# Kernel optimization log

Measured on AMD Instinct MI355X. Metric: run time of the kernel, lower is better.

## Reference

```python
import jax, jax.numpy as jnp
from jax import lax
import numpy as np

VOCAB, TAGS, EMB, HID = 50000, 45, 256, 512
B, S = 32, 256


def setup_inputs() -> dict:
    key = jax.random.key(0)
    ks = jax.random.split(key, 12)
    sc = 0.05
    return {
        "x": jax.random.randint(ks[0], (B, S), 0, VOCAB),
        "tags": jax.random.randint(ks[1], (B, S), 0, TAGS),
        "emb": jax.random.normal(ks[2], (VOCAB, EMB), jnp.float32) * sc,
        "w_ih_f": jax.random.normal(ks[3], (4 * HID, EMB), jnp.float32) * sc,
        "w_hh_f": jax.random.normal(ks[4], (4 * HID, HID), jnp.float32) * sc,
        "b_f": jnp.zeros((4 * HID,), jnp.float32),
        "w_ih_b": jax.random.normal(ks[5], (4 * HID, EMB), jnp.float32) * sc,
        "w_hh_b": jax.random.normal(ks[6], (4 * HID, HID), jnp.float32) * sc,
        "b_b": jnp.zeros((4 * HID,), jnp.float32),
        "lin_w": jax.random.normal(ks[7], (TAGS, 2 * HID), jnp.float32) * sc,
        "lin_b": jnp.zeros((TAGS,), jnp.float32),
        "start_t": jax.random.normal(ks[8], (TAGS,), jnp.float32) * 0.1,
        "end_t": jax.random.normal(ks[9], (TAGS,), jnp.float32) * 0.1,
        "trans": jax.random.normal(ks[10], (TAGS,), jnp.float32)[:, None] * 0.0 + jax.random.normal(ks[11], (TAGS, TAGS), jnp.float32) * 0.1,
    }


def _lstm_dir(xs, w_ih, w_hh, b, reverse):
    # xs: [B,S,E]. PyTorch gate order: i, f, g, o.
    Bsz = xs.shape[0]
    H = w_hh.shape[1]
    def step(carry, x_t):
        h, c = carry
        g = x_t @ w_ih.T + h @ w_hh.T + b
        i, f, gg, o = jnp.split(g, 4, axis=-1)
        c = jax.nn.sigmoid(f) * c + jax.nn.sigmoid(i) * jnp.tanh(gg)
        h = jax.nn.sigmoid(o) * jnp.tanh(c)
        return (h, c), h
    init = (jnp.zeros((Bsz, H), xs.dtype), jnp.zeros((Bsz, H), xs.dtype))
    _, hs = lax.scan(step, init, jnp.swapaxes(xs, 0, 1), reverse=reverse)
    return jnp.swapaxes(hs, 0, 1)  # [B,S,H]


def _crf_nll(em, tags, start_t, end_t, trans):
    # em: [B,S,T]; numerator: score of gold path
    em_sc = jnp.take_along_axis(em, tags[..., None], axis=2)[..., 0].sum(axis=1)
    tr_sc = trans[tags[:, :-1], tags[:, 1:]].sum(axis=1)
    score = start_t[tags[:, 0]] + em_sc + tr_sc + end_t[tags[:, -1]]
    # partition function via forward algorithm (logsumexp recurrence)
    alpha0 = start_t + em[:, 0]  # [B,T]
    def step(alpha, e_t):
        alpha = jax.nn.logsumexp(alpha[:, :, None] + trans[None], axis=1) + e_t
        return alpha, None
    alpha, _ = lax.scan(step, alpha0, jnp.swapaxes(em[:, 1:], 0, 1))
    logZ = jax.nn.logsumexp(alpha + end_t, axis=1)
    return -(score - logZ).mean()  # reduction='mean', loss = -llh


def reference(x, tags, emb, w_ih_f, w_hh_f, b_f, w_ih_b, w_hh_b, b_b,
              lin_w, lin_b, start_t, end_t, trans):
    embeds = emb[x]                               # [B,S,E]
    h_f = _lstm_dir(embeds, w_ih_f, w_hh_f, b_f, False)
    h_b = _lstm_dir(embeds, w_ih_b, w_hh_b, b_b, True)
    lstm_out = jnp.concatenate([h_f, h_b], axis=-1)  # [B,S,2H]
    emissions = lstm_out @ lin_w.T + lin_b           # [B,S,T]
    return _crf_nll(emissions, tags, start_t, end_t, trans)
```

## Files before the change

kernel.cpp:

```cpp
#include <hip/hip_runtime.h>

#define BB 32
#define SS 256
#define EMBD 256
#define HIDD 512
#define NTAG 45
#define TPAD 48
#define NBLK 16
#define APAD 520
#define GRID_REC 32
#define GSTR 130
#define SENT 0x01010101u

typedef __bf16 bf16x8 __attribute__((ext_vector_type(8)));
typedef float  f32x4  __attribute__((ext_vector_type(4)));
typedef short  s16x8  __attribute__((ext_vector_type(8)));
typedef unsigned u32x4 __attribute__((ext_vector_type(4)));

__device__ __forceinline__ unsigned short f2bf(float x) {
  unsigned u = __builtin_bit_cast(unsigned, x);
  u = (u + 0x7fffu + ((u >> 16) & 1u)) >> 16;
  return (unsigned short)u;
}
__device__ __forceinline__ float bf2f(unsigned short u) {
  unsigned v = ((unsigned)u) << 16; return __builtin_bit_cast(float, v);
}
__device__ __forceinline__ float fsig(float x) {
  float e = __builtin_amdgcn_exp2f(-1.44269504f * x);
  return __builtin_amdgcn_rcpf(1.f + e);
}
__device__ __forceinline__ float ftanh(float x) {
  float e = __builtin_amdgcn_exp2f(-2.88539008f * x);
  return 2.f * __builtin_amdgcn_rcpf(1.f + e) - 1.f;
}

__device__ __forceinline__ void st64_sys(unsigned* p, unsigned a, unsigned b) {
  unsigned long long v = ((unsigned long long)b << 32) | (unsigned long long)a;
  asm volatile("global_store_dwordx2 %0, %1, off sc0 sc1" :: "v"(p), "v"(v) : "memory");
}

#define LD8(CPOL)                                                           \
  asm volatile("global_load_dwordx4 %0, %[q0], off " CPOL "\n\t"            \
               "global_load_dwordx4 %1, %[q1], off " CPOL "\n\t"            \
               "global_load_dwordx4 %2, %[q2], off " CPOL "\n\t"            \
               "global_load_dwordx4 %3, %[q3], off " CPOL "\n\t"            \
               "global_load_dwordx4 %4, %[q4], off " CPOL "\n\t"            \
               "global_load_dwordx4 %5, %[q5], off " CPOL "\n\t"            \
               "global_load_dwordx4 %6, %[q6], off " CPOL "\n\t"            \
               "global_load_dwordx4 %7, %[q7], off " CPOL "\n\t"            \
               "s_waitcnt vmcnt(0)"                                         \
               : "=&v"(v0), "=&v"(v1), "=&v"(v2), "=&v"(v3),                \
                 "=&v"(v4), "=&v"(v5), "=&v"(v6), "=&v"(v7)                 \
               : [q0] "v"(p), [q1] "v"(p + 2048), [q2] "v"(p + 4096),       \
                 [q3] "v"(p + 6144), [q4] "v"(p + 8192), [q5] "v"(p + 10240),\
                 [q6] "v"(p + 12288), [q7] "v"(p + 14336)                   \
               : "memory")

__global__ void k_pack_e(const int* __restrict__ x, const float* __restrict__ emb,
                         unsigned short* __restrict__ E) {
  int idx = blockIdx.x * 256 + threadIdx.x;
  int e = idx & 255; int bt = idx >> 8; int b = bt & 31; int t = bt >> 5;
  int tok = x[b * SS + t];
  E[idx] = f2bf(emb[(long)tok * EMBD + e]);
}

__global__ void k_pack_w(const float* __restrict__ wih_f, const float* __restrict__ whh_f,
                         const float* __restrict__ bf_,  const float* __restrict__ wih_b,
                         const float* __restrict__ whh_b, const float* __restrict__ bb_,
                         unsigned short* __restrict__ Wh, unsigned short* __restrict__ Wie,
                         float* __restrict__ Bh) {
  long idx = (long)blockIdx.x * 256 + threadIdx.x;
  int k = (int)(idx % 768); long rest = idx / 768;
  int r2 = (int)(rest & 2047); int dir = (int)(rest >> 11);
  int blk = r2 >> 6, rl = r2 & 63, gate = rl >> 4, hl = rl & 15;
  int orig = gate * HIDD + blk * 16 + hl;
  const float* wih = dir ? wih_b : wih_f;
  const float* whh = dir ? whh_b : whh_f;
  if (k < HIDD) Wh[((long)(dir * 2048 + r2)) * 512 + k] = f2bf(whh[(long)orig * HIDD + k]);
  else          Wie[((long)(dir * 2048 + r2)) * 256 + (k - 512)] = f2bf(wih[(long)orig * EMBD + (k - 512)]);
  if (k == 0) {
    const float* bias = dir ? bb_ : bf_;
    Bh[dir * 2048 + r2] = bias[orig];
  }
}

__global__ void k_pack_l(const float* __restrict__ lin_w, const float* __restrict__ lin_b,
                         unsigned short* __restrict__ LW, float* __restrict__ LB) {
  int idx = blockIdx.x * 256 + threadIdx.x;
  if (idx < TPAD * 1024) {
    int tag = idx >> 10; int c = idx & 1023;
    LW[idx] = (tag < NTAG) ? f2bf(lin_w[tag * 1024 + c]) : (unsigned short)0;
  } else if (idx < TPAD * 1024 + TPAD) {
    int tag = idx - TPAD * 1024;
    LB[tag] = (tag < NTAG) ? lin_b[tag] : 0.f;
  }
}

__launch_bounds__(256)
__global__ void k_eproj(const unsigned short* __restrict__ E,
                        const unsigned short* __restrict__ Wie,
                        const float* __restrict__ Bh,
                        unsigned short* __restrict__ Ep) {
  __shared__ unsigned short W2[64 * 264];
  const int bx = blockIdx.x;
  const int tg = bx & 63, blk = (bx >> 6) & 31, dir = bx >> 11;
  const int tid = threadIdx.x;
  const int w = tid >> 6, lane = tid & 63;
  const int lm = lane & 15, quad = lane >> 4;

  {
    const unsigned short* src = Wie + ((long)(dir * 2048 + blk * 64)) * 256;
    for (int i = 0; i < 8; ++i) {
      int c = i * 256 + tid;
      int row = c >> 5, off = c & 31;
      *(s16x8*)&W2[row * 264 + off * 8] = *(const s16x8*)&src[row * 256 + off * 8];
    }
  }
  __syncthreads();

  f32x4 acc[2][4] = {};
#pragma unroll
  for (int kk = 0; kk < 8; ++kk) {
    s16x8 av[2];
#pragma unroll
    for (int sub = 0; sub < 2; ++sub)
      av[sub] = *(const s16x8*)&E[((long)(tg * 128 + w * 32 + sub * 16 + lm)) * 256 + kk * 32 + quad * 8];
#pragma unroll
    for (int sub = 0; sub < 2; ++sub)
#pragma unroll
      for (int n = 0; n < 4; ++n) {
        s16x8 bs = *(const s16x8*)&W2[(n * 16 + lm) * 264 + kk * 32 + quad * 8];
        acc[sub][n] = __builtin_amdgcn_mfma_f32_16x16x32_bf16(
            __builtin_bit_cast(bf16x8, av[sub]), __builtin_bit_cast(bf16x8, bs), acc[sub][n], 0, 0, 0);
      }
  }
  float bh[4];
#pragma unroll
  for (int n = 0; n < 4; ++n) bh[n] = Bh[dir * 2048 + blk * 64 + n * 16 + lm];
#pragma unroll
  for (int sub = 0; sub < 2; ++sub)
#pragma unroll
    for (int n = 0; n < 4; ++n)
#pragma unroll
      for (int r = 0; r < 4; ++r) {
        int m = w * 32 + sub * 16 + quad * 4 + r;
        int t = tg * 4 + (m >> 5), b = m & 31;
        int row_l = n * 16 + lm;
        Ep[((((long)(dir * 32 + blk) * 256 + t) * 32 + b) * 64) + row_l] =
            f2bf(acc[sub][n][r] + bh[n]);
      }
}

__launch_bounds__(256, 1)
__global__ void k_rec(const unsigned short* __restrict__ Wh,
                      const unsigned short* __restrict__ Ep,
                      unsigned short* __restrict__ H) {
  __shared__ unsigned short A_ls[32 * APAD];
  __shared__ float G_ls[32 * GSTR];

  const int bx = blockIdx.x;
  const int dir = bx & 1;
  const int blk = bx >> 1;
  const int tid = threadIdx.x;
  const int w = tid >> 6, lane = tid & 63;
  const int lm = lane & 15, quad = lane >> 4;

  s16x8 wb[2][16];
  {
    const unsigned short* wsrc =
        Wh + ((long)(dir * 2048 + blk * 128 + w * 32 + lm)) * 512 + quad * 8;
#pragma unroll
    for (int ns = 0; ns < 2; ++ns)
#pragma unroll
      for (int kk = 0; kk < 16; ++kk)
        wb[ns][kk] = *(const s16x8*)&wsrc[ns * 16 * 512 + kk * 32];
  }

  const int m_act = tid >> 3, cg = tid & 7;
  float cst[4] = {0.f, 0.f, 0.f, 0.f};

  unsigned short* Hd = H + (long)dir * SS * BB * HIDD;
  const unsigned short* Epw =
      Ep + ((long)(dir * 32 + 2 * blk + (w >> 1)) * 256) * 32 * 64;
  const int ep_col = (w & 1) * 32 + lm;

  for (int t = 0; t < SS; ++t) {
    const int tE = (dir == 0) ? t : (SS - 1 - t);

    unsigned short epv[16];
    {
      const unsigned short* eb = Epw + ((long)tE * 32 + quad * 4) * 64 + ep_col;
#pragma unroll
      for (int mt = 0; mt < 2; ++mt)
#pragma unroll
        for (int ns = 0; ns < 2; ++ns)
#pragma unroll
          for (int r = 0; r < 4; ++r)
            epv[mt * 8 + ns * 4 + r] = eb[(mt * 16 + r) * 64 + ns * 16];
    }

    f32x4 acc[2][2] = {};
    if (t > 0) {
      {
        const int hslot = (dir == 0) ? (t - 1) : (SS - t);
        const unsigned short* p = Hd + (long)hslot * BB * HIDD + w * 512 + lane * 8;
        s16x8 v0, v1, v2, v3, v4, v5, v6, v7;
        unsigned bad;
        do {
          LD8("sc0 sc1");
          u32x4 u0 = __builtin_bit_cast(u32x4, v0), u1 = __builtin_bit_cast(u32x4, v1);
          u32x4 u2 = __builtin_bit_cast(u32x4, v2), u3 = __builtin_bit_cast(u32x4, v3);
          u32x4 u4 = __builtin_bit_cast(u32x4, v4), u5 = __builtin_bit_cast(u32x4, v5);
          u32x4 u6 = __builtin_bit_cast(u32x4, v6), u7 = __builtin_bit_cast(u32x4, v7);
          unsigned b0 = (u0.x == SENT) | (u0.y == SENT) | (u0.z == SENT) | (u0.w == SENT);
          unsigned b1 = (u1.x == SENT) | (u1.y == SENT) | (u1.z == SENT) | (u1.w == SENT);
          unsigned b2 = (u2.x == SENT) | (u2.y == SENT) | (u2.z == SENT) | (u2.w == SENT);
          unsigned b3 = (u3.x == SENT) | (u3.y == SENT) | (u3.z == SENT) | (u3.w == SENT);
          unsigned b4 = (u4.x == SENT) | (u4.y == SENT) | (u4.z == SENT) | (u4.w == SENT);
          unsigned b5 = (u5.x == SENT) | (u5.y == SENT) | (u5.z == SENT) | (u5.w == SENT);
          unsigned b6 = (u6.x == SENT) | (u6.y == SENT) | (u6.z == SENT) | (u6.w == SENT);
          unsigned b7 = (u7.x == SENT) | (u7.y == SENT) | (u7.z == SENT) | (u7.w == SENT);
          bad = (b0 | b1) | (b2 | b3) | ((b4 | b5) | (b6 | b7));
        } while (__builtin_expect(bad != 0u, 0));
        unsigned short* d = &A_ls[w * APAD + lane * 8];
        *(s16x8*)(d + 0 * 2080) = v0; *(s16x8*)(d + 1 * 2080) = v1;
        *(s16x8*)(d + 2 * 2080) = v2; *(s16x8*)(d + 3 * 2080) = v3;
        *(s16x8*)(d + 4 * 2080) = v4; *(s16x8*)(d + 5 * 2080) = v5;
        *(s16x8*)(d + 6 * 2080) = v6; *(s16x8*)(d + 7 * 2080) = v7;
      }
      __syncthreads();
#pragma unroll
      for (int kk = 0; kk < 16; ++kk) {
        s16x8 av0 = *(const s16x8*)&A_ls[(lm)      * APAD + kk * 32 + quad * 8];
        s16x8 av1 = *(const s16x8*)&A_ls[(16 + lm) * APAD + kk * 32 + quad * 8];
        acc[0][0] = __builtin_amdgcn_mfma_f32_16x16x32_bf16(
            __builtin_bit_cast(bf16x8, av0), __builtin_bit_cast(bf16x8, wb[0][kk]), acc[0][0], 0, 0, 0);
        acc[0][1] = __builtin_amdgcn_mfma_f32_16x16x32_bf16(
            __builtin_bit_cast(bf16x8, av0), __builtin_bit_cast(bf16x8, wb[1][kk]), acc[0][1], 0, 0, 0);
        acc[1][0] = __builtin_amdgcn_mfma_f32_16x16x32_bf16(
            __builtin_bit_cast(bf16x8, av1), __builtin_bit_cast(bf16x8, wb[0][kk]), acc[1][0], 0, 0, 0);
        acc[1][1] = __builtin_amdgcn_mfma_f32_16x16x32_bf16(
            __builtin_bit_cast(bf16x8, av1), __builtin_bit_cast(bf16x8, wb[1][kk]), acc[1][1], 0, 0, 0);
      }
    }
#pragma unroll
    for (int mt = 0; mt < 2; ++mt)
#pragma unroll
      for (int ns = 0; ns < 2; ++ns)
#pragma unroll
        for (int r = 0; r < 4; ++r) {
          int mm = mt * 16 + quad * 4 + r;
          G_ls[mm * GSTR + w * 32 + ns * 16 + lm] =
              acc[mt][ns][r] + bf2f(epv[mt * 8 + ns * 4 + r]);
        }
    __syncthreads();
    {
      float hv[4];
#pragma unroll
      for (int j = 0; j < 4; ++j) {
        int c = cg * 4 + j, sub = c >> 4, hl = c & 15;
        const float* gp = &G_ls[m_act * GSTR + sub * 64 + hl];
        float si = fsig(gp[0]);
        float sf = fsig(gp[16]);
        float tg = ftanh(gp[32]);
        float so = fsig(gp[48]);
        cst[j] = sf * cst[j] + si * tg;
        hv[j] = so * ftanh(cst[j]);
      }
      int tslot = (dir == 0) ? t : (SS - 1 - t);
      unsigned d0 = (unsigned)f2bf(hv[0]) | ((unsigned)f2bf(hv[1]) << 16);
      unsigned d1 = (unsigned)f2bf(hv[2]) | ((unsigned)f2bf(hv[3]) << 16);
      st64_sys((unsigned*)&Hd[(long)tslot * BB * HIDD + (long)m_act * HIDD + blk * 32 + cg * 4],
               d0, d1);
    }
  }
}

__launch_bounds__(256)
__global__ void k_emis(const unsigned short* __restrict__ H,
                       const unsigned short* __restrict__ LW,
                       const float* __restrict__ LB,
                       float* __restrict__ EM) {
  const int row0 = blockIdx.x * 32;
  const int tid = threadIdx.x;
  const int w = tid >> 6, lane = tid & 63;
  const int lm = lane & 15, quad = lane >> 4;
  const unsigned short* Hf = H;
  const unsigned short* Hb = H + (long)SS * BB * HIDD;

  for (int tile = w; tile < 6; tile += 4) {
    int mt = tile / 3, nt = tile % 3;
    int arow = row0 + mt * 16 + lm;
    int nrow = nt * 16 + lm;
    f32x4 acc = {0.f, 0.f, 0.f, 0.f};
#pragma unroll 4
    for (int kk = 0; kk < 32; ++kk) {
      int k0 = kk * 32 + quad * 8;
      s16x8 asv = (k0 < HIDD) ? *(const s16x8*)&Hf[(long)arow * HIDD + k0]
                              : *(const s16x8*)&Hb[(long)arow * HIDD + (k0 - HIDD)];
      s16x8 bsv = *(const s16x8*)&LW[nrow * 1024 + k0];
      acc = __builtin_amdgcn_mfma_f32_16x16x32_bf16(
          __builtin_bit_cast(bf16x8, asv), __builtin_bit_cast(bf16x8, bsv), acc, 0, 0, 0);
    }
    float bias = LB[nrow];
#pragma unroll
    for (int r = 0; r < 4; ++r) {
      int mm = row0 + mt * 16 + quad * 4 + r;
      EM[(long)mm * TPAD + nrow] = acc[r] + bias;
    }
  }
}

__global__ void k_crf(const int* __restrict__ tags, const float* __restrict__ start_t,
                      const float* __restrict__ end_t, const float* __restrict__ trans,
                      const float* __restrict__ EM, float* __restrict__ chain) {
  __shared__ float T_ls[NTAG * TPAD];
  __shared__ float ET[48 * 48 + 16];
  __shared__ float P_ls[64];
  const int b = blockIdx.x;
  const int lane = threadIdx.x;
  const int j = lane;

  for (int i = lane; i < NTAG * NTAG; i += 64)
    T_ls[(i / NTAG) * TPAD + (i % NTAG)] = trans[i];
  for (int i = lane; i < 48 * 48 + 16; i += 64) ET[i] = 0.f;
  __syncthreads();

  float Mj = -1e30f;
  if (j < NTAG) {
    for (int i = 0; i < NTAG; ++i) Mj = fmaxf(Mj, T_ls[i * TPAD + j]);
    for (int i = 0; i < NTAG; ++i) ET[i * 48 + j] = __expf(T_ls[i * TPAD + j] - Mj);
  }
  __syncthreads();

  float et[48];
#pragma unroll
  for (int i = 0; i < 48; ++i) et[i] = ET[i * 48 + j];

  float part = 0.f;
  for (int t = lane; t < SS; t += 64) {
    int tg = tags[b * SS + t];
    part += EM[((long)t * BB + b) * TPAD + tg];
    if (t + 1 < SS) part += T_ls[tg * TPAD + tags[b * SS + t + 1]];
    if (t == 0)      part += start_t[tg];
    if (t == SS - 1) part += end_t[tg];
  }
  for (int off = 32; off; off >>= 1) part += __shfl_down(part, off);
  float score = __shfl(part, 0);

  float alpha = (j < NTAG) ? (start_t[j] + EM[(long)b * TPAD + j]) : -1e30f;
  float e_next = (j < NTAG) ? EM[((long)BB + b) * TPAD + j] : 0.f;
  for (int t = 1; t < SS; ++t) {
    float e_cur = e_next;
    if (t < SS - 1) e_next = (j < NTAG) ? EM[((long)(t + 1) * BB + b) * TPAD + j] : 0.f;
    float am = alpha;
#pragma unroll
    for (int off = 32; off; off >>= 1) am = fmaxf(am, __shfl_xor(am, off));
    float p = __expf(alpha - am);
    P_ls[lane] = p;
    __builtin_amdgcn_wave_barrier();
    float s0 = 0.f, s1 = 0.f, s2 = 0.f, s3 = 0.f;
#pragma unroll
    for (int i0 = 0; i0 < 48; i0 += 4) {
      f32x4 pv = *(const f32x4*)&P_ls[i0];
      s0 += pv.x * et[i0];
      s1 += pv.y * et[i0 + 1];
      s2 += pv.z * et[i0 + 2];
      s3 += pv.w * et[i0 + 3];
    }
    __builtin_amdgcn_wave_barrier();
    float s = (s0 + s1) + (s2 + s3);
    float na = am + Mj + __logf(s) + e_cur;
    alpha = (j < NTAG) ? na : -1e30f;
  }
  float v = (j < NTAG) ? (alpha + end_t[j]) : -1e30f;
  float mx = v;
  for (int off = 32; off; off >>= 1) mx = fmaxf(mx, __shfl_xor(mx, off));
  float s = __expf(v - mx);
  for (int off = 32; off; off >>= 1) s += __shfl_xor(s, off);
  if (lane == 0) chain[b] = score - (mx + __logf(s));
}

__global__ void k_fin(const float* __restrict__ chain, float* __restrict__ out) {
  int lane = threadIdx.x;
  float v = (lane < BB) ? chain[lane] : 0.f;
  for (int off = 32; off; off >>= 1) v += __shfl_xor(v, off);
  if (lane == 0) out[0] = -v / (float)BB;
}

extern "C" void kernel_launch(void* const* d_in, const int* in_sizes, int n_in,
                              void* d_out, int out_size, void* d_ws, size_t ws_size,
                              hipStream_t stream) {
  const int*   x      = (const int*)d_in[0];
  const int*   tags   = (const int*)d_in[1];
  const float* emb    = (const float*)d_in[2];
  const float* wih_f  = (const float*)d_in[3];
  const float* whh_f  = (const float*)d_in[4];
  const float* b_f    = (const float*)d_in[5];
  const float* wih_b  = (const float*)d_in[6];
  const float* whh_b  = (const float*)d_in[7];
  const float* b_b    = (const float*)d_in[8];
  const float* lin_w  = (const float*)d_in[9];
  const float* lin_b  = (const float*)d_in[10];
  const float* start_t= (const float*)d_in[11];
  const float* end_t  = (const float*)d_in[12];
  const float* trans  = (const float*)d_in[13];

  char* ws = (char*)d_ws;
  size_t off = 0;
  auto alloc = [&](size_t bytes) {
    void* p = ws + off; off = (off + bytes + 255) & ~(size_t)255; return p;
  };
  unsigned short* E   = (unsigned short*)alloc((size_t)SS * BB * EMBD * 2);
  unsigned short* Wh  = (unsigned short*)alloc((size_t)2 * 2048 * 512 * 2);
  unsigned short* Wie = (unsigned short*)alloc((size_t)2 * 2048 * 256 * 2);
  float*          Bh  = (float*)         alloc((size_t)2 * 2048 * 4);
  unsigned short* Ep  = (unsigned short*)alloc((size_t)2 * 32 * 256 * 32 * 64 * 2);
  unsigned short* H   = (unsigned short*)alloc((size_t)2 * SS * BB * HIDD * 2);
  unsigned short* LW  = (unsigned short*)alloc((size_t)TPAD * 1024 * 2);
  float*          LB  = (float*)         alloc((size_t)TPAD * 4);
  float*          EM  = (float*)         alloc((size_t)SS * BB * TPAD * 4);
  float*          chain = (float*)       alloc((size_t)BB * 4);

  hipMemsetAsync(H, 0x01, (size_t)2 * SS * BB * HIDD * 2, stream);
  k_pack_e<<<dim3((SS * BB * EMBD) / 256), dim3(256), 0, stream>>>(x, emb, E);
  k_pack_w<<<dim3((2 * 2048 * 768) / 256), dim3(256), 0, stream>>>(
      wih_f, whh_f, b_f, wih_b, whh_b, b_b, Wh, Wie, Bh);
  k_pack_l<<<dim3((TPAD * 1024 + TPAD + 255) / 256), dim3(256), 0, stream>>>(
      lin_w, lin_b, LW, LB);
  k_eproj<<<dim3(4096), dim3(256), 0, stream>>>(E, Wie, Bh, Ep);

  void* kargs[] = {&Wh, &Ep, &H};
  hipLaunchCooperativeKernel((const void*)k_rec, dim3(GRID_REC), dim3(256), kargs, 0, stream);

  k_emis<<<dim3((SS * BB) / 32), dim3(256), 0, stream>>>(H, LW, LB, EM);
  k_crf<<<dim3(BB), dim3(64), 0, stream>>>(tags, start_t, end_t, trans, EM, chain);
  k_fin<<<dim3(1), dim3(64), 0, stream>>>(chain, (float*)d_out);
}
```

Baseline: 1.083 ms.

## Fuse input projection into recurrent kernel and merge packing kernels

Removes the separate input-projection kernel and its Ep buffer, and instead computes the x·W_ih product inside each recurrent step from register-resident W_ih slices and the packed embeddings. The hidden-state load is restructured so each wave polls its own A-operand fragments directly from global memory and feeds them into MFMA, which drops the LDS staging and one barrier per step. The gate buffer is double-buffered, and the three pack kernels are merged into one launch. This trades the global Ep round-trip and extra launches for more MFMA work and register pressure on the serial critical path, plus finer-grained sentinel polling.

```diff
diff --git a/kernel.cpp b/kernel.cpp
--- a/kernel.cpp
+++ b/kernel.cpp
@@ -7,7 +7,6 @@
 #define NTAG 45
 #define TPAD 48
 #define NBLK 16
-#define APAD 520
 #define GRID_REC 32
 #define GSTR 130
 #define SENT 0x01010101u
@@ -22,9 +21,6 @@
   u = (u + 0x7fffu + ((u >> 16) & 1u)) >> 16;
   return (unsigned short)u;
 }
-__device__ __forceinline__ float bf2f(unsigned short u) {
-  unsigned v = ((unsigned)u) << 16; return __builtin_bit_cast(float, v);
-}
 __device__ __forceinline__ float fsig(float x) {
   float e = __builtin_amdgcn_exp2f(-1.44269504f * x);
   return __builtin_amdgcn_rcpf(1.f + e);
@@ -33,130 +29,76 @@
   float e = __builtin_amdgcn_exp2f(-2.88539008f * x);
   return 2.f * __builtin_amdgcn_rcpf(1.f + e) - 1.f;
 }
+__device__ __forceinline__ f32x4 MF(s16x8 a, s16x8 b, f32x4 c) {
+  return __builtin_amdgcn_mfma_f32_16x16x32_bf16(
+      __builtin_bit_cast(bf16x8, a), __builtin_bit_cast(bf16x8, b), c, 0, 0, 0);
+}
+__device__ __forceinline__ unsigned has_sent(s16x8 v) {
+  u32x4 u = __builtin_bit_cast(u32x4, v);
+  return (unsigned)((u.x == SENT) | (u.y == SENT) | (u.z == SENT) | (u.w == SENT));
+}
 
 __device__ __forceinline__ void st64_sys(unsigned* p, unsigned a, unsigned b) {
   unsigned long long v = ((unsigned long long)b << 32) | (unsigned long long)a;
   asm volatile("global_store_dwordx2 %0, %1, off sc0 sc1" :: "v"(p), "v"(v) : "memory");
 }
-
-#define LD8(CPOL)                                                           \
-  asm volatile("global_load_dwordx4 %0, %[q0], off " CPOL "\n\t"            \
-               "global_load_dwordx4 %1, %[q1], off " CPOL "\n\t"            \
-               "global_load_dwordx4 %2, %[q2], off " CPOL "\n\t"            \
-               "global_load_dwordx4 %3, %[q3], off " CPOL "\n\t"            \
-               "global_load_dwordx4 %4, %[q4], off " CPOL "\n\t"            \
-               "global_load_dwordx4 %5, %[q5], off " CPOL "\n\t"            \
-               "global_load_dwordx4 %6, %[q6], off " CPOL "\n\t"            \
-               "global_load_dwordx4 %7, %[q7], off " CPOL "\n\t"            \
-               "s_waitcnt vmcnt(0)"                                         \
-               : "=&v"(v0), "=&v"(v1), "=&v"(v2), "=&v"(v3),                \
-                 "=&v"(v4), "=&v"(v5), "=&v"(v6), "=&v"(v7)                 \
-               : [q0] "v"(p), [q1] "v"(p + 2048), [q2] "v"(p + 4096),       \
-                 [q3] "v"(p + 6144), [q4] "v"(p + 8192), [q5] "v"(p + 10240),\
-                 [q6] "v"(p + 12288), [q7] "v"(p + 14336)                   \
-               : "memory")
-
-__global__ void k_pack_e(const int* __restrict__ x, const float* __restrict__ emb,
-                         unsigned short* __restrict__ E) {
-  int idx = blockIdx.x * 256 + threadIdx.x;
-  int e = idx & 255; int bt = idx >> 8; int b = bt & 31; int t = bt >> 5;
-  int tok = x[b * SS + t];
-  E[idx] = f2bf(emb[(long)tok * EMBD + e]);
-}
-
-__global__ void k_pack_w(const float* __restrict__ wih_f, const float* __restrict__ whh_f,
-                         const float* __restrict__ bf_,  const float* __restrict__ wih_b,
-                         const float* __restrict__ whh_b, const float* __restrict__ bb_,
-                         unsigned short* __restrict__ Wh, unsigned short* __restrict__ Wie,
-                         float* __restrict__ Bh) {
-  long idx = (long)blockIdx.x * 256 + threadIdx.x;
-  int k = (int)(idx % 768); long rest = idx / 768;
-  int r2 = (int)(rest & 2047); int dir = (int)(rest >> 11);
-  int blk = r2 >> 6, rl = r2 & 63, gate = rl >> 4, hl = rl & 15;
-  int orig = gate * HIDD + blk * 16 + hl;
-  const float* wih = dir ? wih_b : wih_f;
-  const float* whh = dir ? whh_b : whh_f;
-  if (k < HIDD) Wh[((long)(dir * 2048 + r2)) * 512 + k] = f2bf(whh[(long)orig * HIDD + k]);
-  else          Wie[((long)(dir * 2048 + r2)) * 256 + (k - 512)] = f2bf(wih[(long)orig * EMBD + (k - 512)]);
-  if (k == 0) {
-    const float* bias = dir ? bb_ : bf_;
-    Bh[dir * 2048 + r2] = bias[orig];
-  }
-}
-
-__global__ void k_pack_l(const float* __restrict__ lin_w, const float* __restrict__ lin_b,
-                         unsigned short* __restrict__ LW, float* __restrict__ LB) {
-  int idx = blockIdx.x * 256 + threadIdx.x;
-  if (idx < TPAD * 1024) {
-    int tag = idx >> 10; int c = idx & 1023;
-    LW[idx] = (tag < NTAG) ? f2bf(lin_w[tag * 1024 + c]) : (unsigned short)0;
-  } else if (idx < TPAD * 1024 + TPAD) {
-    int tag = idx - TPAD * 1024;
-    LB[tag] = (tag < NTAG) ? lin_b[tag] : 0.f;
-  }
-}
-
-__launch_bounds__(256)
-__global__ void k_eproj(const unsigned short* __restrict__ E,
-                        const unsigned short* __restrict__ Wie,
-                        const float* __restrict__ Bh,
-                        unsigned short* __restrict__ Ep) {
-  __shared__ unsigned short W2[64 * 264];
-  const int bx = blockIdx.x;
-  const int tg = bx & 63, blk = (bx >> 6) & 31, dir = bx >> 11;
+#define LDH2()                                                          \
+  asm volatile("global_load_dwordx4 %0, %2, off sc0 sc1\n\t"            \
+               "global_load_dwordx4 %1, %3, off sc0 sc1\n\t"            \
+               "s_waitcnt vmcnt(0)"                                     \
+               : "=&v"(a0), "=&v"(a1) : "v"(p0), "v"(p1) : "memory")
+
+#define NB_W 12288
+#define NB_E 8192
+#define NB_L 193
+__global__ void k_pack(const int* __restrict__ x, const float* __restrict__ emb,
+                       const float* __restrict__ wih_f, const float* __restrict__ whh_f,
+                       const float* __restrict__ bf_,  const float* __restrict__ wih_b,
+                       const float* __restrict__ whh_b, const float* __restrict__ bb_,
+                       const float* __restrict__ lin_w, const float* __restrict__ lin_b,
+                       unsigned short* __restrict__ E,  unsigned short* __restrict__ Wh,
+                       unsigned short* __restrict__ Wie, float* __restrict__ Bh,
+                       unsigned short* __restrict__ LW, float* __restrict__ LB) {
+  const int bxg = blockIdx.x;
   const int tid = threadIdx.x;
-  const int w = tid >> 6, lane = tid & 63;
-  const int lm = lane & 15, quad = lane >> 4;
-
-  {
-    const unsigned short* src = Wie + ((long)(dir * 2048 + blk * 64)) * 256;
-    for (int i = 0; i < 8; ++i) {
-      int c = i * 256 + tid;
-      int row = c >> 5, off = c & 31;
-      *(s16x8*)&W2[row * 264 + off * 8] = *(const s16x8*)&src[row * 256 + off * 8];
-    }
-  }
-  __syncthreads();
-
-  f32x4 acc[2][4] = {};
-#pragma unroll
-  for (int kk = 0; kk < 8; ++kk) {
-    s16x8 av[2];
-#pragma unroll
-    for (int sub = 0; sub < 2; ++sub)
-      av[sub] = *(const s16x8*)&E[((long)(tg * 128 + w * 32 + sub * 16 + lm)) * 256 + kk * 32 + quad * 8];
-#pragma unroll
-    for (int sub = 0; sub < 2; ++sub)
-#pragma unroll
-      for (int n = 0; n < 4; ++n) {
-        s16x8 bs = *(const s16x8*)&W2[(n * 16 + lm) * 264 + kk * 32 + quad * 8];
-        acc[sub][n] = __builtin_amdgcn_mfma_f32_16x16x32_bf16(
-            __builtin_bit_cast(bf16x8, av[sub]), __builtin_bit_cast(bf16x8, bs), acc[sub][n], 0, 0, 0);
-      }
-  }
-  float bh[4];
-#pragma unroll
-  for (int n = 0; n < 4; ++n) bh[n] = Bh[dir * 2048 + blk * 64 + n * 16 + lm];
-#pragma unroll
-  for (int sub = 0; sub < 2; ++sub)
-#pragma unroll
-    for (int n = 0; n < 4; ++n)
-#pragma unroll
-      for (int r = 0; r < 4; ++r) {
-        int m = w * 32 + sub * 16 + quad * 4 + r;
-        int t = tg * 4 + (m >> 5), b = m & 31;
-        int row_l = n * 16 + lm;
-        Ep[((((long)(dir * 32 + blk) * 256 + t) * 32 + b) * 64) + row_l] =
-            f2bf(acc[sub][n][r] + bh[n]);
-      }
+  if (bxg < NB_W) {
+    long idx = (long)bxg * 256 + tid;
+    int k = (int)(idx % 768); long rest = idx / 768;
+    int r2 = (int)(rest & 2047); int dir = (int)(rest >> 11);
+    int blk = r2 >> 6, rl = r2 & 63, gate = rl >> 4, hl = rl & 15;
+    int orig = gate * HIDD + blk * 16 + hl;
+    const float* wih = dir ? wih_b : wih_f;
+    const float* whh = dir ? whh_b : whh_f;
+    if (k < HIDD) Wh[((long)(dir * 2048 + r2)) * 512 + k] = f2bf(whh[(long)orig * HIDD + k]);
+    else          Wie[((long)(dir * 2048 + r2)) * 256 + (k - 512)] = f2bf(wih[(long)orig * EMBD + (k - 512)]);
+    if (k == 0) {
+      const float* bias = dir ? bb_ : bf_;
+      Bh[dir * 2048 + r2] = bias[orig];
+    }
+  } else if (bxg < NB_W + NB_E) {
+    int idx = (bxg - NB_W) * 256 + tid;
+    int e = idx & 255; int bt = idx >> 8; int b = bt & 31; int t = bt >> 5;
+    int tok = x[b * SS + t];
+    E[idx] = f2bf(emb[(long)tok * EMBD + e]);
+  } else {
+    int idx = (bxg - NB_W - NB_E) * 256 + tid;
+    if (idx < TPAD * 1024) {
+      int tag = idx >> 10; int c = idx & 1023;
+      LW[idx] = (tag < NTAG) ? f2bf(lin_w[tag * 1024 + c]) : (unsigned short)0;
+    } else if (idx < TPAD * 1024 + TPAD) {
+      int tag = idx - TPAD * 1024;
+      LB[tag] = (tag < NTAG) ? lin_b[tag] : 0.f;
+    }
+  }
 }
 
 __launch_bounds__(256, 1)
 __global__ void k_rec(const unsigned short* __restrict__ Wh,
-                      const unsigned short* __restrict__ Ep,
+                      const unsigned short* __restrict__ Wie,
+                      const float* __restrict__ Bh,
+                      const unsigned short* __restrict__ E,
                       unsigned short* __restrict__ H) {
-  __shared__ unsigned short A_ls[32 * APAD];
-  __shared__ float G_ls[32 * GSTR];
+  __shared__ float G_ls[2][32 * GSTR];
 
   const int bx = blockIdx.x;
   const int dir = bx & 1;
@@ -165,84 +107,64 @@
   const int w = tid >> 6, lane = tid & 63;
   const int lm = lane & 15, quad = lane >> 4;
 
-  s16x8 wb[2][16];
+  s16x8 wb[2][16], wie[2][8];
+  float bh[2];
   {
-    const unsigned short* wsrc =
-        Wh + ((long)(dir * 2048 + blk * 128 + w * 32 + lm)) * 512 + quad * 8;
-#pragma unroll
-    for (int ns = 0; ns < 2; ++ns)
-#pragma unroll
-      for (int kk = 0; kk < 16; ++kk)
-        wb[ns][kk] = *(const s16x8*)&wsrc[ns * 16 * 512 + kk * 32];
+    const long rbase = (long)(dir * 2048 + blk * 128 + w * 32 + lm);
+#pragma unroll
+    for (int ns = 0; ns < 2; ++ns) {
+      const unsigned short* wsrc = Wh + (rbase + ns * 16) * 512 + quad * 8;
+#pragma unroll
+      for (int kk = 0; kk < 16; ++kk) wb[ns][kk] = *(const s16x8*)&wsrc[kk * 32];
+      const unsigned short* wesrc = Wie + (rbase + ns * 16) * 256 + quad * 8;
+#pragma unroll
+      for (int kk = 0; kk < 8; ++kk) wie[ns][kk] = *(const s16x8*)&wesrc[kk * 32];
+      bh[ns] = Bh[rbase + ns * 16];
+    }
   }
 
   const int m_act = tid >> 3, cg = tid & 7;
   float cst[4] = {0.f, 0.f, 0.f, 0.f};
 
   unsigned short* Hd = H + (long)dir * SS * BB * HIDD;
-  const unsigned short* Epw =
-      Ep + ((long)(dir * 32 + 2 * blk + (w >> 1)) * 256) * 32 * 64;
-  const int ep_col = (w & 1) * 32 + lm;
 
   for (int t = 0; t < SS; ++t) {
     const int tE = (dir == 0) ? t : (SS - 1 - t);
-
-    unsigned short epv[16];
+    f32x4 acc[2][2] = {};
+
     {
-      const unsigned short* eb = Epw + ((long)tE * 32 + quad * 4) * 64 + ep_col;
-#pragma unroll
-      for (int mt = 0; mt < 2; ++mt)
-#pragma unroll
-        for (int ns = 0; ns < 2; ++ns)
-#pragma unroll
-          for (int r = 0; r < 4; ++r)
-            epv[mt * 8 + ns * 4 + r] = eb[(mt * 16 + r) * 64 + ns * 16];
-    }
-
-    f32x4 acc[2][2] = {};
+      const unsigned short* eb = E + ((long)tE * BB) * EMBD + quad * 8;
+#pragma unroll
+      for (int kk = 0; kk < 8; ++kk) {
+        s16x8 e0 = *(const s16x8*)&eb[(long)lm * EMBD + kk * 32];
+        s16x8 e1 = *(const s16x8*)&eb[(long)(16 + lm) * EMBD + kk * 32];
+        acc[0][0] = MF(e0, wie[0][kk], acc[0][0]);
+        acc[0][1] = MF(e0, wie[1][kk], acc[0][1]);
+        acc[1][0] = MF(e1, wie[0][kk], acc[1][0]);
+        acc[1][1] = MF(e1, wie[1][kk], acc[1][1]);
+      }
+    }
+
     if (t > 0) {
-      {
-        const int hslot = (dir == 0) ? (t - 1) : (SS - t);
-        const unsigned short* p = Hd + (long)hslot * BB * HIDD + w * 512 + lane * 8;
-        s16x8 v0, v1, v2, v3, v4, v5, v6, v7;
-        unsigned bad;
-        do {
-          LD8("sc0 sc1");
-          u32x4 u0 = __builtin_bit_cast(u32x4, v0), u1 = __builtin_bit_cast(u32x4, v1);
-          u32x4 u2 = __builtin_bit_cast(u32x4, v2), u3 = __builtin_bit_cast(u32x4, v3);
-          u32x4 u4 = __builtin_bit_cast(u32x4, v4), u5 = __builtin_bit_cast(u32x4, v5);
-          u32x4 u6 = __builtin_bit_cast(u32x4, v6), u7 = __builtin_bit_cast(u32x4, v7);
-          unsigned b0 = (u0.x == SENT) | (u0.y == SENT) | (u0.z == SENT) | (u0.w == SENT);
-          unsigned b1 = (u1.x == SENT) | (u1.y == SENT) | (u1.z == SENT) | (u1.w == SENT);
-          unsigned b2 = (u2.x == SENT) | (u2.y == SENT) | (u2.z == SENT) | (u2.w == SENT);
-          unsigned b3 = (u3.x == SENT) | (u3.y == SENT) | (u3.z == SENT) | (u3.w == SENT);
-          unsigned b4 = (u4.x == SENT) | (u4.y == SENT) | (u4.z == SENT) | (u4.w == SENT);
-          unsigned b5 = (u5.x == SENT) | (u5.y == SENT) | (u5.z == SENT) | (u5.w == SENT);
-          unsigned b6 = (u6.x == SENT) | (u6.y == SENT) | (u6.z == SENT) | (u6.w == SENT);
-          unsigned b7 = (u7.x == SENT) | (u7.y == SENT) | (u7.z == SENT) | (u7.w == SENT);
-          bad = (b0 | b1) | (b2 | b3) | ((b4 | b5) | (b6 | b7));
-        } while (__builtin_expect(bad != 0u, 0));
-        unsigned short* d = &A_ls[w * APAD + lane * 8];
-        *(s16x8*)(d + 0 * 2080) = v0; *(s16x8*)(d + 1 * 2080) = v1;
-        *(s16x8*)(d + 2 * 2080) = v2; *(s16x8*)(d + 3 * 2080) = v3;
-        *(s16x8*)(d + 4 * 2080) = v4; *(s16x8*)(d + 5 * 2080) = v5;
-        *(s16x8*)(d + 6 * 2080) = v6; *(s16x8*)(d + 7 * 2080) = v7;
+      const int hslot = (dir == 0) ? (t - 1) : (SS - t);
+      const unsigned short* hb = Hd + (long)hslot * BB * HIDD + quad * 8;
+#pragma unroll 4
+      for (int kk = 0; kk < 16; ++kk) {
+        const unsigned short* p0 = hb + (long)lm * HIDD + kk * 32;
+        const unsigned short* p1 = hb + (long)(16 + lm) * HIDD + kk * 32;
+        s16x8 a0, a1;
+        for (;;) {
+          LDH2();
+          if (!(has_sent(a0) | has_sent(a1))) break;
+        }
+        acc[0][0] = MF(a0, wb[0][kk], acc[0][0]);
+        acc[0][1] = MF(a0, wb[1][kk], acc[0][1]);
+        acc[1][0] = MF(a1, wb[0][kk], acc[1][0]);
+        acc[1][1] = MF(a1, wb[1][kk], acc[1][1]);
       }
-      __syncthreads();
-#pragma unroll
-      for (int kk = 0; kk < 16; ++kk) {
-        s16x8 av0 = *(const s16x8*)&A_ls[(lm)      * APAD + kk * 32 + quad * 8];
-        s16x8 av1 = *(const s16x8*)&A_ls[(16 + lm) * APAD + kk * 32 + quad * 8];
-        acc[0][0] = __builtin_amdgcn_mfma_f32_16x16x32_bf16(
-            __builtin_bit_cast(bf16x8, av0), __builtin_bit_cast(bf16x8, wb[0][kk]), acc[0][0], 0, 0, 0);
-        acc[0][1] = __builtin_amdgcn_mfma_f32_16x16x32_bf16(
-            __builtin_bit_cast(bf16x8, av0), __builtin_bit_cast(bf16x8, wb[1][kk]), acc[0][1], 0, 0, 0);
-        acc[1][0] = __builtin_amdgcn_mfma_f32_16x16x32_bf16(
-            __builtin_bit_cast(bf16x8, av1), __builtin_bit_cast(bf16x8, wb[0][kk]), acc[1][0], 0, 0, 0);
-        acc[1][1] = __builtin_amdgcn_mfma_f32_16x16x32_bf16(
-            __builtin_bit_cast(bf16x8, av1), __builtin_bit_cast(bf16x8, wb[1][kk]), acc[1][1], 0, 0, 0);
-      }
-    }
+    }
+
+    float* G = G_ls[t & 1];
 #pragma unroll
     for (int mt = 0; mt < 2; ++mt)
 #pragma unroll
@@ -250,8 +172,7 @@
 #pragma unroll
         for (int r = 0; r < 4; ++r) {
           int mm = mt * 16 + quad * 4 + r;
-          G_ls[mm * GSTR + w * 32 + ns * 16 + lm] =
-              acc[mt][ns][r] + bf2f(epv[mt * 8 + ns * 4 + r]);
+          G[mm * GSTR + w * 32 + ns * 16 + lm] = acc[mt][ns][r] + bh[ns];
         }
     __syncthreads();
     {
@@ -259,7 +180,7 @@
 #pragma unroll
       for (int j = 0; j < 4; ++j) {
         int c = cg * 4 + j, sub = c >> 4, hl = c & 15;
-        const float* gp = &G_ls[m_act * GSTR + sub * 64 + hl];
+        const float* gp = &G[m_act * GSTR + sub * 64 + hl];
         float si = fsig(gp[0]);
         float sf = fsig(gp[16]);
         float tg = ftanh(gp[32]);
@@ -415,7 +336,6 @@
   unsigned short* Wh  = (unsigned short*)alloc((size_t)2 * 2048 * 512 * 2);
   unsigned short* Wie = (unsigned short*)alloc((size_t)2 * 2048 * 256 * 2);
   float*          Bh  = (float*)         alloc((size_t)2 * 2048 * 4);
-  unsigned short* Ep  = (unsigned short*)alloc((size_t)2 * 32 * 256 * 32 * 64 * 2);
   unsigned short* H   = (unsigned short*)alloc((size_t)2 * SS * BB * HIDD * 2);
   unsigned short* LW  = (unsigned short*)alloc((size_t)TPAD * 1024 * 2);
   float*          LB  = (float*)         alloc((size_t)TPAD * 4);
@@ -423,14 +343,11 @@
   float*          chain = (float*)       alloc((size_t)BB * 4);
 
   hipMemsetAsync(H, 0x01, (size_t)2 * SS * BB * HIDD * 2, stream);
-  k_pack_e<<<dim3((SS * BB * EMBD) / 256), dim3(256), 0, stream>>>(x, emb, E);
-  k_pack_w<<<dim3((2 * 2048 * 768) / 256), dim3(256), 0, stream>>>(
-      wih_f, whh_f, b_f, wih_b, whh_b, b_b, Wh, Wie, Bh);
-  k_pack_l<<<dim3((TPAD * 1024 + TPAD + 255) / 256), dim3(256), 0, stream>>>(
-      lin_w, lin_b, LW, LB);
-  k_eproj<<<dim3(4096), dim3(256), 0, stream>>>(E, Wie, Bh, Ep);
-
-  void* kargs[] = {&Wh, &Ep, &H};
+  k_pack<<<dim3(NB_W + NB_E + NB_L), dim3(256), 0, stream>>>(
+      x, emb, wih_f, whh_f, b_f, wih_b, whh_b, b_b, lin_w, lin_b,
+      E, Wh, Wie, Bh, LW, LB);
+
+  void* kargs[] = {&Wh, &Wie, &Bh, &E, &H};
   hipLaunchCooperativeKernel((const void*)k_rec, dim3(GRID_REC), dim3(256), kargs, 0, stream);
 
   k_emis<<<dim3((SS * BB) / 32), dim3(256), 0, stream>>>(H, LW, LB, EM);
```

New measurement: 3.243 ms. 199% more time.
